# Optimization experiments

Measured on AMD Instinct MI355X. Metric: run time of the kernel, lower is better.

## Reference

```python
import jax, jax.numpy as jnp
import numpy as np

B, T, D_IN = 64, 365, 10
D_MODEL, N_HEAD, D_K = 256, 16, 8
D_HEAD = D_MODEL // N_HEAD  # 16, value head dim
MAX_POS = 365 + 2 * 30      # max_position + 2*max_temporal_shift = 425
BN_EPS = 1e-5


def _pos_table(n_pos, d, temp=1000.0):
    # standard sinusoidal table (frozen in the original via Embedding.from_pretrained)
    pos = np.arange(n_pos)[:, None].astype(np.float64)
    i = np.arange(d)[None, :]
    angle = pos / np.power(temp, 2 * (i // 2) / d)
    tab = np.where(i % 2 == 0, np.sin(angle), np.cos(angle))
    return jnp.asarray(tab, jnp.float32)

POS_TABLE = _pos_table(MAX_POS, D_MODEL)


def _linear_layer(x, W, b, g, beta):
    # LinearLayer = Linear -> BatchNorm1d (train-mode batch stats, per-feature) -> ReLU
    y = x @ W.T + b
    ax = tuple(range(y.ndim - 1))
    mu = y.mean(ax, keepdims=True)
    var = y.var(ax, keepdims=True)  # biased var, matches torch BN
    y = (y - mu) * jax.lax.rsqrt(var + BN_EPS) * g + beta
    return jax.nn.relu(y)


def _forward(positions, x, w1, b1, g1, e1, w2, b2, g2, e2, w3, b3, g3, e3,
             ws1, ws2, wi, bi, gi, ei, wk, bk, wq, bq, wm, bm, gm, em,
             wd1, bd1, gd1, ed1, wd2, bd2, gd2, ed2, wc, bc):
    # channel MLP encoder: 10 -> 64 -> 128 -> 256
    out = _linear_layer(x, w1, b1, g1, e1)
    out = _linear_layer(out, w2, b2, g2, e2)
    out = _linear_layer(out, w3, b3, g3, e3)                    # [B,T,256]
    # channel SE attention: avgpool over time, 2 linears (no bias), sigmoid, residual
    pooled = out.mean(axis=1, keepdims=True)                     # [B,1,256]
    att = jax.nn.sigmoid(jax.nn.relu(pooled @ ws1.T) @ ws2.T)    # [B,1,256]
    out = att * pooled + out                                     # broadcast residual
    # temporal attention block
    h = _linear_layer(out, wi, bi, gi, ei)                       # inconv -> [B,T,256]
    e = h + POS_TABLE[positions]                                 # add positional encoding
    q = (e @ wq.T + bq).reshape(B, T, N_HEAD, D_K)
    k = (e @ wk.T + bk).reshape(B, T, N_HEAD, D_K)
    v = e.reshape(B, T, N_HEAD, D_HEAD)
    # 'cross' attention: full score matrix, mean over key dim, softmax over query dim
    scores = jnp.einsum('bthd,bshd->bhts', q, k) / jnp.sqrt(jnp.float32(D_K))  # [B,H,T,T]
    scores = scores.mean(axis=-1)                                # [B,H,T]
    a = jax.nn.softmax(scores, axis=-1)                          # [B,H,T]
    y = jnp.einsum('bht,bthe->bhe', a, v).reshape(B, D_MODEL)    # [B,256]
    y = _linear_layer(y, wm, bm, gm, em)                         # mlp 256 -> 128
    # decoder: 128 -> 64 -> 32 -> num_classes
    z = _linear_layer(y, wd1, bd1, gd1, ed1)
    z = _linear_layer(z, wd2, bd2, gd2, ed2)
    return z @ wc.T + bc                                         # logits [B,10]


def setup_inputs():
    key = jax.random.key(0)
    ks = jax.random.split(key, 16)
    n = lambda i, sh: jax.random.normal(ks[i], sh, jnp.float32) * 0.05
    z, o = jnp.zeros, jnp.ones
    return {
        'x': jax.random.normal(ks[0], (B, T, D_IN), jnp.float32),
        'positions': jnp.sort(jax.random.randint(ks[1], (B, T), 0, MAX_POS), axis=-1),
        'w1': n(2, (64, D_IN)), 'b1': z(64), 'g1': o(64), 'e1': z(64),
        'w2': n(3, (128, 64)), 'b2': z(128), 'g2': o(128), 'e2': z(128),
        'w3': n(4, (256, 128)), 'b3': z(256), 'g3': o(256), 'e3': z(256),
        'ws1': n(5, (16, 256)), 'ws2': n(6, (256, 16)),
        'wi': n(7, (256, 256)), 'bi': z(256), 'gi': o(256), 'ei': z(256),
        'wk': n(8, (128, 256)), 'bk': z(128),
        'wq': n(9, (128, 256)), 'bq': z(128),
        'wm': n(10, (128, 256)), 'bm': z(128), 'gm': o(128), 'em': z(128),
        'wd1': n(11, (64, 128)), 'bd1': z(64), 'gd1': o(64), 'ed1': z(64),
        'wd2': n(12, (32, 64)), 'bd2': z(32), 'gd2': o(32), 'ed2': z(32),
        'wc': n(13, (10, 32)), 'bc': z(10),
    }


def reference(x, positions, w1, b1, g1, e1, w2, b2, g2, e2, w3, b3, g3, e3,
              ws1, ws2, wi, bi, gi, ei, wk, bk, wq, bq, wm, bm, gm, em,
              wd1, bd1, gd1, ed1, wd2, bd2, gd2, ed2, wc, bc):
    return _forward(positions, x, w1, b1, g1, e1, w2, b2, g2, e2, w3, b3, g3, e3,
                    ws1, ws2, wi, bi, gi, ei, wk, bk, wq, bq, wm, bm, gm, em,
                    wd1, bd1, gd1, ed1, wd2, bd2, gd2, ed2, wc, bc)
```

## Files before the change

kernel.cpp:

```cpp
#include <hip/hip_runtime.h>
#include <hip/hip_bf16.h>
#include <math.h>

#define TT 365
#define BT 23360
#define NPOS 425

typedef __hip_bfloat16 bf16;
typedef __attribute__((ext_vector_type(8))) short s16x8;
typedef __attribute__((ext_vector_type(4))) float f32x4;

__device__ __forceinline__ float b2f(bf16 v) { return __bfloat162float(v); }
__device__ __forceinline__ bf16  f2b(float v) { return __float2bfloat16(v); }
__device__ __forceinline__ float u2f(unsigned u) { return __uint_as_float(u); }
__device__ __forceinline__ short f2bs(float v) { bf16 h = __float2bfloat16(v); return *reinterpret_cast<short*>(&h); }
__device__ __forceinline__ void unpack8(uint4 raw, float* v) {
    v[0] = u2f(raw.x << 16); v[1] = u2f(raw.x & 0xffff0000u);
    v[2] = u2f(raw.y << 16); v[3] = u2f(raw.y & 0xffff0000u);
    v[4] = u2f(raw.z << 16); v[5] = u2f(raw.z & 0xffff0000u);
    v[6] = u2f(raw.w << 16); v[7] = u2f(raw.w & 0xffff0000u);
}

__global__ __launch_bounds__(256) void prep_kernel(
    float* __restrict__ stats, float* __restrict__ pooled, float* __restrict__ esum,
    const float* __restrict__ w2, const float* __restrict__ w3, const float* __restrict__ wi,
    const float* __restrict__ wq,
    bf16* __restrict__ whi, bf16* __restrict__ wlo, float* __restrict__ tab)
{
    int i = blockIdx.x * 256 + threadIdx.x;
    if (i < 2048)  { stats[i] = 0.f; return; }  i -= 2048;
    if (i < 16384) { pooled[i] = 0.f; return; } i -= 16384;
    if (i < 16384) { esum[i] = 0.f; return; }   i -= 16384;
    if (i < 139264) {
        float w;
        if      (i < 8192)   w = w2[i];
        else if (i < 40960)  w = w3[i - 8192];
        else if (i < 106496) w = wi[i - 40960];
        else                 w = wq[i - 106496];
        bf16 h = f2b(w);
        whi[i] = h;
        wlo[i] = f2b(w - b2f(h));
        return;
    } i -= 139264;
    if (i < 108800) {
        int c = i & 255, p = i >> 8;
        float e = (float)(2 * (c >> 1)) * (1.f / 256.f);
        float ang = (float)p * exp2f(-e * 9.96578428466209f);
        tab[i] = (c & 1) ? cosf(ang) : sinf(ang);
    }
}

__global__ __launch_bounds__(256) void gemm_l1_kernel(
    const float* __restrict__ x,
    const float* __restrict__ W, const float* __restrict__ bias,
    bf16* __restrict__ Y, float* __restrict__ stats)
{
    const int t  = threadIdx.x;
    const int tx = t & 15, ty = t >> 4;
    const int row0 = blockIdx.x * 64;
    __shared__ float As[64][17];
    __shared__ float Ws[16][65];
    __shared__ float red_s[4][64];
    __shared__ float red_q[4][64];
    float acc[4][4];
#pragma unroll
    for (int rr = 0; rr < 4; ++rr)
#pragma unroll
        for (int cc = 0; cc < 4; ++cc) acc[rr][cc] = 0.f;
#pragma unroll
    for (int i = 0; i < 4; ++i) {
        int idx = t + i * 256, r = idx >> 4, c = idx & 15;
        As[r][c] = (c < 10) ? x[(size_t)(row0 + r) * 10 + c] : 0.f;
    }
#pragma unroll
    for (int i = 0; i < 4; ++i) {
        int idx = t + i * 256, c = idx >> 4, kk = idx & 15;
        Ws[kk][c] = (kk < 10) ? W[(size_t)c * 10 + kk] : 0.f;
    }
    __syncthreads();
#pragma unroll
    for (int kk = 0; kk < 10; ++kk) {
        float a[4];
#pragma unroll
        for (int rr = 0; rr < 4; ++rr) a[rr] = As[ty * 4 + rr][kk];
#pragma unroll
        for (int cc = 0; cc < 4; ++cc) {
            float w = Ws[kk][cc * 16 + tx];
#pragma unroll
            for (int rr = 0; rr < 4; ++rr) acc[rr][cc] = fmaf(a[rr], w, acc[rr][cc]);
        }
    }
    float s_cc[4], q_cc[4];
#pragma unroll
    for (int cc = 0; cc < 4; ++cc) { s_cc[cc] = 0.f; q_cc[cc] = 0.f; }
#pragma unroll
    for (int rr = 0; rr < 4; ++rr) {
        int row = row0 + ty * 4 + rr;
#pragma unroll
        for (int cc = 0; cc < 4; ++cc) {
            int col = cc * 16 + tx;
            float v = acc[rr][cc] + bias[col];
            Y[(size_t)row * 64 + col] = f2b(v);
            s_cc[cc] += v; q_cc[cc] += v * v;
        }
    }
    int w = t >> 6;
#pragma unroll
    for (int cc = 0; cc < 4; ++cc) {
        float s = s_cc[cc], q = q_cc[cc];
        s += __shfl_xor(s, 16); q += __shfl_xor(q, 16);
        s += __shfl_xor(s, 32); q += __shfl_xor(q, 32);
        if ((t & 63) < 16) { red_s[w][cc * 16 + tx] = s; red_q[w][cc * 16 + tx] = q; }
    }
    __syncthreads();
    if (t < 64) {
        float s = red_s[0][t] + red_s[1][t] + red_s[2][t] + red_s[3][t];
        float q = red_q[0][t] + red_q[1][t] + red_q[2][t] + red_q[3][t];
        atomicAdd(&stats[t], s);
        atomicAdd(&stats[256 + t], q);
    }
}

template<int MODE, int K>
__global__ __launch_bounds__(256) void mfma_gemm(
    const bf16* __restrict__ A,
    const bf16* __restrict__ Whi, const bf16* __restrict__ Wlo,
    const float* __restrict__ bias,
    bf16* __restrict__ Y, int ldY, float* __restrict__ stats,
    const float* __restrict__ bnstats, const float* __restrict__ bng,
    const float* __restrict__ bnb, const float* __restrict__ sebuf)
{
    constexpr int KC = (K > 128) ? 128 : K;
    __shared__ s16x8 Wl[2][KC / 8][64];
    __shared__ float red_s[4][64];
    __shared__ float red_q[4][64];
    __shared__ float scb[MODE ? K : 1];
    __shared__ float shb[MODE ? K : 1];
    const int t = threadIdx.x, wave = t >> 6, lane = t & 63;
    const int n16 = lane & 15, quad = lane >> 4;
    const int m0 = blockIdx.x * 64 + wave * 16;
    const int col0 = blockIdx.y * 64;
    const int sc_ = t & 63, skg0 = t >> 6;
    const bf16* gh = Whi + (size_t)(col0 + sc_) * K;
    const bf16* gl = Wlo + (size_t)(col0 + sc_) * K;
#pragma unroll
    for (int kg = skg0; kg < KC / 8; kg += 4) {
        Wl[0][kg][sc_] = *(const s16x8*)(gh + kg * 8);
        Wl[1][kg][sc_] = *(const s16x8*)(gl + kg * 8);
    }
    if (MODE) {
        if (t < K) {
            float mu = bnstats[t] * (1.f / (float)BT);
            float var = bnstats[256 + t] * (1.f / (float)BT) - mu * mu;
            float sc = rsqrtf(var + 1e-5f) * bng[t];
            scb[t] = sc; shb[t] = bnb[t] - mu * sc;
        }
    }
    __syncthreads();
    const int arow = m0 + n16;
    const float* sev = (MODE == 2) ? (sebuf + (arow / TT) * 256) : nullptr;
    const bf16* Ap = A + (size_t)arow * K + quad * 8;
    s16x8 af[K / 32];
#pragma unroll
    for (int i = 0; i < K / 32; ++i) {
        s16x8 raw = *(const s16x8*)(Ap + i * 32);
        if (MODE) {
            int kb = i * 32 + quad * 8;
#pragma unroll
            for (int j = 0; j < 8; ++j) {
                float y = u2f(((unsigned)(unsigned short)raw[j]) << 16);
                float v = fmaxf(fmaf(y, scb[kb + j], shb[kb + j]), 0.f);
                if (MODE == 2) v += sev[kb + j];
                raw[j] = f2bs(v);
            }
        }
        af[i] = raw;
    }
    f32x4 acc[4];
    f32x4 zero = {0.f, 0.f, 0.f, 0.f};
#pragma unroll
    for (int ct = 0; ct < 4; ++ct) acc[ct] = zero;
#pragma unroll
    for (int kc = 0; kc < K; kc += KC) {
        if (kc) {
            __syncthreads();
#pragma unroll
            for (int kg = skg0; kg < KC / 8; kg += 4) {
                Wl[0][kg][sc_] = *(const s16x8*)(gh + kc + kg * 8);
                Wl[1][kg][sc_] = *(const s16x8*)(gl + kc + kg * 8);
            }
            __syncthreads();
        }
#pragma unroll
        for (int i = 0; i < KC / 32; ++i) {
            const int kgq = i * 4 + quad;
            const s16x8 a = af[(kc >> 5) + i];
#pragma unroll
            for (int ct = 0; ct < 4; ++ct) {
                s16x8 bl = Wl[1][kgq][ct * 16 + n16];
                s16x8 bh = Wl[0][kgq][ct * 16 + n16];
                acc[ct] = __builtin_amdgcn_mfma_f32_16x16x32_bf16(a, bl, acc[ct], 0, 0, 0);
                acc[ct] = __builtin_amdgcn_mfma_f32_16x16x32_bf16(a, bh, acc[ct], 0, 0, 0);
            }
        }
    }
#pragma unroll
    for (int ct = 0; ct < 4; ++ct) {
        int col = col0 + ct * 16 + n16;
        float bv = bias[col];
        float s = 0.f, q = 0.f;
#pragma unroll
        for (int r = 0; r < 4; ++r) {
            float v = acc[ct][r] + bv;
            int row = m0 + quad * 4 + r;
            Y[(size_t)row * ldY + col] = f2b(v);
            s += v; q += v * v;
        }
        s += __shfl_xor(s, 16); q += __shfl_xor(q, 16);
        s += __shfl_xor(s, 32); q += __shfl_xor(q, 32);
        if (quad == 0) { red_s[wave][ct * 16 + n16] = s; red_q[wave][ct * 16 + n16] = q; }
    }
    if (stats) {
        __syncthreads();
        if (t < 64) {
            float s = red_s[0][t] + red_s[1][t] + red_s[2][t] + red_s[3][t];
            float q = red_q[0][t] + red_q[1][t] + red_q[2][t] + red_q[3][t];
            atomicAdd(&stats[col0 + t], s);
            atomicAdd(&stats[256 + col0 + t], q);
        }
    }
}

__global__ __launch_bounds__(256) void pool_partial_kernel(
    const bf16* __restrict__ Y3, const float* __restrict__ stats,
    const float* __restrict__ g3, const float* __restrict__ e3,
    float* __restrict__ pooled)
{
    const int b = blockIdx.x, part = blockIdx.y, t = threadIdx.x;
    const int cg = t & 31, rs = t >> 5;
    __shared__ float scb[256], shb[256];
    __shared__ float pp[8][256];
    {
        float mu = stats[t] * (1.f / (float)BT);
        float var = stats[256 + t] * (1.f / (float)BT) - mu * mu;
        float sc = rsqrtf(var + 1e-5f) * g3[t];
        scb[t] = sc; shb[t] = e3[t] - mu * sc;
    }
    __syncthreads();
    float acc[8] = {0.f,0.f,0.f,0.f,0.f,0.f,0.f,0.f};
    const int r0 = part * 46;
#pragma unroll
    for (int i = 0; i < 6; ++i) {
        int l = rs + i * 8;
        int r = r0 + l;
        if (l < 46 && r < TT) {
            uint4 raw = *(const uint4*)(Y3 + ((size_t)b * TT + r) * 256 + cg * 8);
            float v[8];
            unpack8(raw, v);
#pragma unroll
            for (int j = 0; j < 8; ++j)
                acc[j] += fmaxf(fmaf(v[j], scb[cg * 8 + j], shb[cg * 8 + j]), 0.f);
        }
    }
#pragma unroll
    for (int j = 0; j < 8; ++j) pp[rs][cg * 8 + j] = acc[j];
    __syncthreads();
    float s = 0.f;
#pragma unroll
    for (int r = 0; r < 8; ++r) s += pp[r][t];
    atomicAdd(&pooled[b * 256 + t], s);
}

__global__ __launch_bounds__(256) void se_mlp_kernel(const float* __restrict__ pooled,
                                                     const float* __restrict__ ws1,
                                                     const float* __restrict__ ws2,
                                                     float* __restrict__ se) {
    int b = blockIdx.x, f = threadIdx.x;
    __shared__ float pl[256];
    __shared__ float hidden[16];
    float p = pooled[b * 256 + f] * (1.f / (float)TT);
    pl[f] = p;
    __syncthreads();
    if (f < 16) {
        float h = 0.f;
        for (int k2 = 0; k2 < 256; ++k2) h = fmaf(pl[k2], ws1[f * 256 + k2], h);
        hidden[f] = fmaxf(h, 0.f);
    }
    __syncthreads();
    float a = 0.f;
    for (int k2 = 0; k2 < 16; ++k2) a = fmaf(hidden[k2], ws2[f * 16 + k2], a);
    a = 1.f / (1.f + expf(-a));
    se[b * 256 + f] = a * p;
}

__global__ __launch_bounds__(256) void bnrelu8_kernel(
    const bf16* __restrict__ Y, const float* __restrict__ stats,
    const float* __restrict__ g, const float* __restrict__ beta,
    bf16* __restrict__ Out, const float* __restrict__ tab, const int* __restrict__ pos,
    float* __restrict__ esum) {
    __shared__ float pe[8][256];
    const int t = threadIdx.x;
    int i = (blockIdx.x * 256 + t) * 8;
    int col = i & 255, row = i >> 8;
    uint4 raw = *(const uint4*)(Y + i);
    float v[8];
    unpack8(raw, v);
    const float invM = 1.f / (float)BT;
    const float* tr = tab + pos[row] * 256 + col;
    bf16 tmp[8] __attribute__((aligned(16)));
    float* pr = &pe[t >> 5][col];
#pragma unroll
    for (int j = 0; j < 8; ++j) {
        float mu  = stats[col + j] * invM;
        float var = stats[256 + col + j] * invM - mu * mu;
        float o = (v[j] - mu) * rsqrtf(var + 1e-5f) * g[col + j] + beta[col + j];
        float ev = fmaxf(o, 0.f) + tr[j];
        tmp[j] = f2b(ev);
        pr[j] = ev;
    }
    *(uint4*)(Out + i) = *(const uint4*)tmp;
    __syncthreads();
    const int g0 = blockIdx.x * 8;
    const int b0 = g0 / TT, b1 = (g0 + 7) / TT;
    const int split = (b1 != b0) ? (b1 * TT - g0) : 8;
    float s0 = 0.f, s1 = 0.f;
#pragma unroll
    for (int rr = 0; rr < 8; ++rr) {
        float vv = pe[rr][t];
        if (rr < split) s0 += vv; else s1 += vv;
    }
    atomicAdd(&esum[b0 * 256 + t], s0);
    if (b1 != b0) atomicAdd(&esum[b1 * 256 + t], s1);
}

__global__ __launch_bounds__(64) void attn3_kernel(
    const bf16* __restrict__ e, const float* __restrict__ esum,
    const float* __restrict__ wk, const float* __restrict__ bk,
    const float* __restrict__ wq, const float* __restrict__ bq,
    float* __restrict__ yv)
{
    __shared__ float kqL[256];
    __shared__ float aw[368];
    const int b = blockIdx.x, h = blockIdx.y;
    const int lane = threadIdx.x;
    float4 es = *(const float4*)(esum + b * 256 + lane * 4);
    float ks[8];
#pragma unroll
    for (int d = 0; d < 8; ++d) {
        float4 wv = *(const float4*)(wk + (size_t)(h * 8 + d) * 256 + lane * 4);
        ks[d] = es.x * wv.x + es.y * wv.y + es.z * wv.z + es.w * wv.w;
    }
#pragma unroll
    for (int off = 1; off < 64; off <<= 1)
#pragma unroll
        for (int d = 0; d < 8; ++d) ks[d] += __shfl_xor(ks[d], off);
#pragma unroll
    for (int d = 0; d < 8; ++d) ks[d] += (float)TT * bk[h * 8 + d];
    {
        float4 kq = {0.f, 0.f, 0.f, 0.f};
#pragma unroll
        for (int d = 0; d < 8; ++d) {
            float4 wv = *(const float4*)(wq + (size_t)(h * 8 + d) * 256 + lane * 4);
            kq.x = fmaf(ks[d], wv.x, kq.x);
            kq.y = fmaf(ks[d], wv.y, kq.y);
            kq.z = fmaf(ks[d], wv.z, kq.z);
            kq.w = fmaf(ks[d], wv.w, kq.w);
        }
        *(float4*)&kqL[lane * 4] = kq;
    }
    float cb = 0.f;
#pragma unroll
    for (int d = 0; d < 8; ++d) cb = fmaf(ks[d], bq[h * 8 + d], cb);
    __syncthreads();
    const int gp = lane >> 3, gl = lane & 7;
    float4 kr[8];
    {
        const float4* kq4 = (const float4*)(kqL + gl * 32);
#pragma unroll
        for (int u = 0; u < 8; ++u) kr[u] = kq4[u];
    }
    const float scale = 1.f / (sqrtf(8.f) * (float)TT);
    const bf16* ebs = e + (size_t)b * TT * 256 + gl * 32;
    for (int it = 0; it < 46; ++it) {
        int r = it * 8 + gp;
        if (r < TT) {
            const bf16* ep = ebs + (size_t)r * 256;
            float dot = 0.f;
#pragma unroll
            for (int u = 0; u < 4; ++u) {
                uint4 raw = *(const uint4*)(ep + u * 8);
                float v[8];
                unpack8(raw, v);
                float4 ka = kr[u * 2], kb2 = kr[u * 2 + 1];
                dot += v[0] * ka.x + v[1] * ka.y + v[2] * ka.z + v[3] * ka.w
                     + v[4] * kb2.x + v[5] * kb2.y + v[6] * kb2.z + v[7] * kb2.w;
            }
            dot += __shfl_xor(dot, 1);
            dot += __shfl_xor(dot, 2);
            dot += __shfl_xor(dot, 4);
            if (gl == 0) aw[r] = (dot + cb) * scale;
        }
    }
    __syncthreads();
    float sv[6];
    float m = -1e30f;
#pragma unroll
    for (int i = 0; i < 6; ++i) {
        int r = lane + i * 64;
        sv[i] = (r < TT) ? aw[r] : -1e30f;
        m = fmaxf(m, sv[i]);
    }
#pragma unroll
    for (int off = 1; off < 64; off <<= 1) m = fmaxf(m, __shfl_xor(m, off));
    float sum = 0.f;
#pragma unroll
    for (int i = 0; i < 6; ++i) {
        float ev = (sv[i] > -1e29f) ? expf(sv[i] - m) : 0.f;
        sv[i] = ev; sum += ev;
    }
#pragma unroll
    for (int off = 1; off < 64; off <<= 1) sum += __shfl_xor(sum, off);
    float inv = 1.f / sum;
#pragma unroll
    for (int i = 0; i < 6; ++i) {
        int r = lane + i * 64;
        if (r < TT) aw[r] = sv[i] * inv;
    }
    __syncthreads();
    const int half = lane & 1, rs = lane >> 1;
    float acc[8] = {0.f,0.f,0.f,0.f,0.f,0.f,0.f,0.f};
    const bf16* ebase = e + (size_t)b * TT * 256 + h * 16 + half * 8;
#pragma unroll
    for (int i = 0; i < 12; ++i) {
        int r = rs + i * 32;
        if (r < TT) {
            uint4 raw = *(const uint4*)(ebase + (size_t)r * 256);
            float v[8];
            unpack8(raw, v);
            float a = aw[r];
#pragma unroll
            for (int j = 0; j < 8; ++j) acc[j] = fmaf(a, v[j], acc[j]);
        }
    }
#pragma unroll
    for (int off = 2; off < 64; off <<= 1)
#pragma unroll
        for (int j = 0; j < 8; ++j) acc[j] += __shfl_xor(acc[j], off);
    if (lane < 2) {
        float* op = yv + b * 256 + h * 16 + half * 8;
#pragma unroll
        for (int j = 0; j < 8; ++j) op[j] = acc[j];
    }
}


__global__ __launch_bounds__(256) void tail_m_kernel(
    const float* __restrict__ yv, const float* __restrict__ wm,
    const float* __restrict__ gm, const float* __restrict__ em,
    float* __restrict__ z1)
{
    __shared__ float Xq[4160];
    const int t = threadIdx.x, r = t & 63, cw = t >> 6;
    const int c0 = blockIdx.x * 8 + cw * 2;
    const float4* wf4 = (const float4*)wm;
    float acc[2] = {0.f, 0.f};
    for (int p = 0; p < 4; ++p) {
        if (p) __syncthreads();
        for (int i = t; i < 4096; i += 256) {
            int kk = i & 63, rr = i >> 6;
            Xq[kk * 65 + rr] = yv[rr * 256 + p * 64 + kk];
        }
        __syncthreads();
#pragma unroll 4
        for (int k4 = 0; k4 < 16; ++k4) {
            float xv[4];
#pragma unroll
            for (int j = 0; j < 4; ++j) xv[j] = Xq[(k4 * 4 + j) * 65 + r];
#pragma unroll
            for (int c = 0; c < 2; ++c) {
                float4 w = wf4[(c0 + c) * 64 + p * 16 + k4];
                acc[c] = fmaf(xv[0], w.x, acc[c]);
                acc[c] = fmaf(xv[1], w.y, acc[c]);
                acc[c] = fmaf(xv[2], w.z, acc[c]);
                acc[c] = fmaf(xv[3], w.w, acc[c]);
            }
        }
    }
#pragma unroll
    for (int c = 0; c < 2; ++c) {
        float v = acc[c];
        float s = v, q = v * v;
#pragma unroll
        for (int off = 1; off < 64; off <<= 1) { s += __shfl_xor(s, off); q += __shfl_xor(q, off); }
        float mu = s * (1.f / 64.f), var = q * (1.f / 64.f) - mu * mu;
        float sc = rsqrtf(var + 1e-5f) * gm[c0 + c], sh = em[c0 + c] - mu * sc;
        z1[r * 128 + c0 + c] = fmaxf(fmaf(v, sc, sh), 0.f);
    }
}

__global__ __launch_bounds__(256) void tail_d1_kernel(
    const float* __restrict__ z1, const float* __restrict__ wd1,
    const float* __restrict__ gd1, const float* __restrict__ ed1,
    float* __restrict__ z2)
{
    __shared__ float Xq[4160];
    const int t = threadIdx.x, r = t & 63, cw = t >> 6;
    const int c0 = blockIdx.x * 8 + cw * 2;
    const float4* wf4 = (const float4*)wd1;
    float acc[2] = {0.f, 0.f};
    for (int p = 0; p < 2; ++p) {
        if (p) __syncthreads();
        for (int i = t; i < 4096; i += 256) {
            int kk = i & 63, rr = i >> 6;
            Xq[kk * 65 + rr] = z1[rr * 128 + p * 64 + kk];
        }
        __syncthreads();
#pragma unroll 4
        for (int k4 = 0; k4 < 16; ++k4) {
            float xv[4];
#pragma unroll
            for (int j = 0; j < 4; ++j) xv[j] = Xq[(k4 * 4 + j) * 65 + r];
#pragma unroll
            for (int c = 0; c < 2; ++c) {
                float4 w = wf4[(c0 + c) * 32 + p * 16 + k4];
                acc[c] = fmaf(xv[0], w.x, acc[c]);
                acc[c] = fmaf(xv[1], w.y, acc[c]);
                acc[c] = fmaf(xv[2], w.z, acc[c]);
                acc[c] = fmaf(xv[3], w.w, acc[c]);
            }
        }
    }
#pragma unroll
    for (int c = 0; c < 2; ++c) {
        float v = acc[c];
        float s = v, q = v * v;
#pragma unroll
        for (int off = 1; off < 64; off <<= 1) { s += __shfl_xor(s, off); q += __shfl_xor(q, off); }
        float mu = s * (1.f / 64.f), var = q * (1.f / 64.f) - mu * mu;
        float sc = rsqrtf(var + 1e-5f) * gd1[c0 + c], sh = ed1[c0 + c] - mu * sc;
        z2[r * 64 + c0 + c] = fmaxf(fmaf(v, sc, sh), 0.f);
    }
}

__global__ __launch_bounds__(256) void tail_d2c_kernel(
    const float* __restrict__ z2, const float* __restrict__ wd2,
    const float* __restrict__ gd2, const float* __restrict__ ed2,
    const float* __restrict__ wc, const float* __restrict__ bc,
    float* __restrict__ out)
{
    __shared__ float Xq[4160];
    __shared__ float Z3t[2048];
    __shared__ float WcL[320];
    const int t = threadIdx.x, r = t & 63, cw = t >> 6;
    const int c03 = cw * 8;
    for (int i = t; i < 4096; i += 256) {
        int kk = i & 63, rr = i >> 6;
        Xq[kk * 65 + rr] = z2[rr * 64 + kk];
    }
    if (t < 80) ((float4*)WcL)[t] = ((const float4*)wc)[t];
    __syncthreads();
    const float4* wf4 = (const float4*)wd2;
    float acc[8] = {0.f,0.f,0.f,0.f,0.f,0.f,0.f,0.f};
#pragma unroll 4
    for (int k4 = 0; k4 < 16; ++k4) {
        float xv[4];
#pragma unroll
        for (int j = 0; j < 4; ++j) xv[j] = Xq[(k4 * 4 + j) * 65 + r];
#pragma unroll
        for (int c = 0; c < 8; ++c) {
            float4 w = wf4[(c03 + c) * 16 + k4];
            acc[c] = fmaf(xv[0], w.x, acc[c]);
            acc[c] = fmaf(xv[1], w.y, acc[c]);
            acc[c] = fmaf(xv[2], w.z, acc[c]);
            acc[c] = fmaf(xv[3], w.w, acc[c]);
        }
    }
#pragma unroll
    for (int c = 0; c < 8; ++c) {
        float v = acc[c];
        float s = v, q = v * v;
#pragma unroll
        for (int off = 1; off < 64; off <<= 1) { s += __shfl_xor(s, off); q += __shfl_xor(q, off); }
        float mu = s * (1.f / 64.f), var = q * (1.f / 64.f) - mu * mu;
        float sc = rsqrtf(var + 1e-5f) * gd2[c03 + c], sh = ed2[c03 + c] - mu * sc;
        Z3t[(c03 + c) * 64 + r] = fmaxf(fmaf(v, sc, sh), 0.f);
    }
    __syncthreads();
#pragma unroll
    for (int i = 0; i < 3; ++i) {
        int idx = t + i * 256;
        if (idx < 640) {
            int rr = idx / 10, c = idx - rr * 10;
            float s = bc[c];
#pragma unroll
            for (int kk = 0; kk < 32; ++kk) s = fmaf(Z3t[kk * 64 + rr], WcL[c * 32 + kk], s);
            out[idx] = s;
        }
    }
}


extern "C" void kernel_launch(void* const* d_in, const int* in_sizes, int n_in,
                              void* d_out, int out_size, void* d_ws, size_t ws_size,
                              hipStream_t stream) {
    (void)in_sizes; (void)n_in; (void)out_size; (void)ws_size;
    const float* x  = (const float*)d_in[0];
    const int* pos  = (const int*)d_in[1];
    const float *w1 = (const float*)d_in[2],  *b1 = (const float*)d_in[3],
                *g1 = (const float*)d_in[4],  *e1 = (const float*)d_in[5];
    const float *w2 = (const float*)d_in[6],  *b2 = (const float*)d_in[7],
                *g2 = (const float*)d_in[8],  *e2 = (const float*)d_in[9];
    const float *w3 = (const float*)d_in[10], *b3 = (const float*)d_in[11],
                *g3 = (const float*)d_in[12], *e3 = (const float*)d_in[13];
    const float *ws1 = (const float*)d_in[14], *ws2 = (const float*)d_in[15];
    const float *wi = (const float*)d_in[16], *bi = (const float*)d_in[17],
                *gi = (const float*)d_in[18], *ei = (const float*)d_in[19];
    const float *wk = (const float*)d_in[20], *bk = (const float*)d_in[21];
    const float *wq = (const float*)d_in[22], *bq = (const float*)d_in[23];
    const float *wm = (const float*)d_in[24], *bm = (const float*)d_in[25],
                *gm = (const float*)d_in[26], *em = (const float*)d_in[27];
    const float *wd1 = (const float*)d_in[28], *bd1 = (const float*)d_in[29],
                *gd1 = (const float*)d_in[30], *ed1 = (const float*)d_in[31];
    const float *wd2 = (const float*)d_in[32], *bd2 = (const float*)d_in[33],
                *gd2 = (const float*)d_in[34], *ed2 = (const float*)d_in[35];
    const float *wc = (const float*)d_in[36], *bc = (const float*)d_in[37];
    float* out = (float*)d_out;
    (void)bm; (void)bd1; (void)bd2;

    char* w8 = (char*)d_ws;
    bf16*  actA   = (bf16*)(w8);
    bf16*  actB   = (bf16*)(w8 + 11960320);
    bf16*  whi    = (bf16*)(w8 + 23920640);
    bf16*  wlo    = (bf16*)(w8 + 24199168);
    float* tab    = (float*)(w8 + 24477696);
    float* stats  = (float*)(w8 + 24912896);
    float* pooled = (float*)(w8 + 24921088);
    float* sebuf  = (float*)(w8 + 24986624);
    float* esum   = (float*)(w8 + 25052160);
    float* yvb    = (float*)(w8 + 25117696);
    float* z1     = esum;
    float* z2     = sebuf;

    prep_kernel<<<1105, 256, 0, stream>>>(stats, pooled, esum, w2, w3, wi, wq, whi, wlo, tab);
    gemm_l1_kernel<<<365, 256, 0, stream>>>(x, w1, b1, actB, stats);
    mfma_gemm<1, 64><<<dim3(365, 2), 256, 0, stream>>>(actB, whi, wlo, b2,
                                                       actA, 128, stats + 512, stats, g1, e1, nullptr);
    mfma_gemm<1, 128><<<dim3(365, 4), 256, 0, stream>>>(actA, whi + 8192, wlo + 8192, b3,
                                                        actB, 256, stats + 1024, stats + 512, g2, e2, nullptr);
    pool_partial_kernel<<<dim3(64, 8), 256, 0, stream>>>(actB, stats + 1024, g3, e3, pooled);
    se_mlp_kernel<<<64, 256, 0, stream>>>(pooled, ws1, ws2, sebuf);
    mfma_gemm<2, 256><<<dim3(365, 4), 256, 0, stream>>>(actB, whi + 40960, wlo + 40960, bi,
                                                        actA, 256, stats + 1536, stats + 1024, g3, e3, sebuf);
    bnrelu8_kernel<<<BT * 256 / 2048, 256, 0, stream>>>(actA, stats + 1536, gi, ei, actB, tab, pos, esum);
    attn3_kernel<<<dim3(64, 16), 64, 0, stream>>>(actB, esum, wk, bk, wq, bq, yvb);
    tail_m_kernel<<<16, 256, 0, stream>>>(yvb, wm, gm, em, z1);
    tail_d1_kernel<<<8, 256, 0, stream>>>(z1, wd1, gd1, ed1, z2);
    tail_d2c_kernel<<<1, 256, 0, stream>>>(z2, wd2, gd2, ed2, wc, bc, out);
}
```

Baseline: 316.9 us.

## Pre-tile split-bf16 weights for coalesced LDS loads and XCD-aware block remap

The prep kernel now writes the hi/lo bf16 weight copies in a tiled layout, with each 64-column by 8-k group stored contiguously. This lets the MFMA GEMM fill shared memory with a flat, fully coalesced copy instead of strided per-row loads. The GEMM launch moves to a 1D grid, and block ids are remapped so consecutive logical tiles land on the same XCD, aiming for better L2 reuse of A rows and weights. It also stops converting wq, which the GEMM path does not use, shrinking the prep grid.

```diff
diff --git a/kernel.cpp b/kernel.cpp
--- a/kernel.cpp
+++ b/kernel.cpp
@@ -24,24 +24,23 @@
 __global__ __launch_bounds__(256) void prep_kernel(
     float* __restrict__ stats, float* __restrict__ pooled, float* __restrict__ esum,
     const float* __restrict__ w2, const float* __restrict__ w3, const float* __restrict__ wi,
-    const float* __restrict__ wq,
     bf16* __restrict__ whi, bf16* __restrict__ wlo, float* __restrict__ tab)
 {
     int i = blockIdx.x * 256 + threadIdx.x;
     if (i < 2048)  { stats[i] = 0.f; return; }  i -= 2048;
     if (i < 16384) { pooled[i] = 0.f; return; } i -= 16384;
     if (i < 16384) { esum[i] = 0.f; return; }   i -= 16384;
-    if (i < 139264) {
-        float w;
-        if      (i < 8192)   w = w2[i];
-        else if (i < 40960)  w = w3[i - 8192];
-        else if (i < 106496) w = wi[i - 40960];
-        else                 w = wq[i - 106496];
+    if (i < 106496) {
+        float w; int out, k, Kq, base;
+        if (i < 8192)       { int j = i;         Kq = 64;  out = j >> 6; k = j & 63;  base = 0;     w = w2[j]; }
+        else if (i < 40960) { int j = i - 8192;  Kq = 128; out = j >> 7; k = j & 127; base = 8192;  w = w3[j]; }
+        else                { int j = i - 40960; Kq = 256; out = j >> 8; k = j & 255; base = 40960; w = wi[j]; }
+        int P = base + ((out >> 6) * (Kq >> 3) + (k >> 3)) * 512 + (out & 63) * 8 + (k & 7);
         bf16 h = f2b(w);
-        whi[i] = h;
-        wlo[i] = f2b(w - b2f(h));
+        whi[P] = h;
+        wlo[P] = f2b(w - b2f(h));
         return;
-    } i -= 139264;
+    } i -= 106496;
     if (i < 108800) {
         int c = i & 255, p = i >> 8;
         float e = (float)(2 * (c >> 1)) * (1.f / 256.f);
@@ -121,7 +120,7 @@
     }
 }
 
-template<int MODE, int K>
+template<int MODE, int K, int NCB>
 __global__ __launch_bounds__(256) void mfma_gemm(
     const bf16* __restrict__ A,
     const bf16* __restrict__ Whi, const bf16* __restrict__ Wlo,
@@ -131,6 +130,7 @@
     const float* __restrict__ bnb, const float* __restrict__ sebuf)
 {
     constexpr int KC = (K > 128) ? 128 : K;
+    constexpr int VPC = (KC / 8) * 64;
     __shared__ s16x8 Wl[2][KC / 8][64];
     __shared__ float red_s[4][64];
     __shared__ float red_q[4][64];
@@ -138,15 +138,20 @@
     __shared__ float shb[MODE ? K : 1];
     const int t = threadIdx.x, wave = t >> 6, lane = t & 63;
     const int n16 = lane & 15, quad = lane >> 4;
-    const int m0 = blockIdx.x * 64 + wave * 16;
-    const int col0 = blockIdx.y * 64;
-    const int sc_ = t & 63, skg0 = t >> 6;
-    const bf16* gh = Whi + (size_t)(col0 + sc_) * K;
-    const bf16* gl = Wlo + (size_t)(col0 + sc_) * K;
-#pragma unroll
-    for (int kg = skg0; kg < KC / 8; kg += 4) {
-        Wl[0][kg][sc_] = *(const s16x8*)(gh + kg * 8);
-        Wl[1][kg][sc_] = *(const s16x8*)(gl + kg * 8);
+    constexpr int nwg = 365 * NCB;
+    constexpr int sq = nwg >> 3, sr = nwg & 7;
+    const int xcd = blockIdx.x & 7, sidx = blockIdx.x >> 3;
+    const int L = (xcd < sr ? xcd * (sq + 1) : sr * (sq + 1) + (xcd - sr) * sq) + sidx;
+    const int rowblk = L / NCB, colblk = L - rowblk * NCB;
+    const int m0 = rowblk * 64 + wave * 16;
+    const int col0 = colblk * 64;
+    const s16x8* gH = (const s16x8*)Whi + (size_t)colblk * (K >> 3) * 64;
+    const s16x8* gL = (const s16x8*)Wlo + (size_t)colblk * (K >> 3) * 64;
+    s16x8* WlF = (s16x8*)Wl;
+#pragma unroll
+    for (int idx = t; idx < VPC; idx += 256) {
+        WlF[idx]       = gH[idx];
+        WlF[VPC + idx] = gL[idx];
     }
     if (MODE) {
         if (t < K) {
@@ -185,9 +190,9 @@
         if (kc) {
             __syncthreads();
 #pragma unroll
-            for (int kg = skg0; kg < KC / 8; kg += 4) {
-                Wl[0][kg][sc_] = *(const s16x8*)(gh + kc + kg * 8);
-                Wl[1][kg][sc_] = *(const s16x8*)(gl + kc + kg * 8);
+            for (int idx = t; idx < VPC; idx += 256) {
+                WlF[idx]       = gH[(kc >> 3) * 64 + idx];
+                WlF[VPC + idx] = gL[(kc >> 3) * 64 + idx];
             }
             __syncthreads();
         }
@@ -641,16 +646,16 @@
     float* z1     = esum;
     float* z2     = sebuf;
 
-    prep_kernel<<<1105, 256, 0, stream>>>(stats, pooled, esum, w2, w3, wi, wq, whi, wlo, tab);
+    prep_kernel<<<977, 256, 0, stream>>>(stats, pooled, esum, w2, w3, wi, whi, wlo, tab);
     gemm_l1_kernel<<<365, 256, 0, stream>>>(x, w1, b1, actB, stats);
-    mfma_gemm<1, 64><<<dim3(365, 2), 256, 0, stream>>>(actB, whi, wlo, b2,
-                                                       actA, 128, stats + 512, stats, g1, e1, nullptr);
-    mfma_gemm<1, 128><<<dim3(365, 4), 256, 0, stream>>>(actA, whi + 8192, wlo + 8192, b3,
-                                                        actB, 256, stats + 1024, stats + 512, g2, e2, nullptr);
+    mfma_gemm<1, 64, 2><<<730, 256, 0, stream>>>(actB, whi, wlo, b2,
+                                                 actA, 128, stats + 512, stats, g1, e1, nullptr);
+    mfma_gemm<1, 128, 4><<<1460, 256, 0, stream>>>(actA, whi + 8192, wlo + 8192, b3,
+                                                   actB, 256, stats + 1024, stats + 512, g2, e2, nullptr);
     pool_partial_kernel<<<dim3(64, 8), 256, 0, stream>>>(actB, stats + 1024, g3, e3, pooled);
     se_mlp_kernel<<<64, 256, 0, stream>>>(pooled, ws1, ws2, sebuf);
-    mfma_gemm<2, 256><<<dim3(365, 4), 256, 0, stream>>>(actB, whi + 40960, wlo + 40960, bi,
-                                                        actA, 256, stats + 1536, stats + 1024, g3, e3, sebuf);
+    mfma_gemm<2, 256, 4><<<1460, 256, 0, stream>>>(actB, whi + 40960, wlo + 40960, bi,
+                                                   actA, 256, stats + 1536, stats + 1024, g3, e3, sebuf);
     bnrelu8_kernel<<<BT * 256 / 2048, 256, 0, stream>>>(actA, stats + 1536, gi, ei, actB, tab, pos, esum);
     attn3_kernel<<<dim3(64, 16), 64, 0, stream>>>(actB, esum, wk, bk, wq, bq, yvb);
     tail_m_kernel<<<16, 256, 0, stream>>>(yvb, wm, gm, em, z1);
```

New measurement: 295.6 us. 1.07x faster.
